# Kernel optimization log

Measured on AMD Instinct MI355X. Metric: run time of the kernel, lower is better.

## Reference

```python
import jax, jax.numpy as jnp
import numpy as np

WINDOW = 5  # pairs (i, j) with j in [i+1, i+5]
NEG = -1e30


def setup_inputs() -> dict:
    key = jax.random.key(0)
    k1, k2, k3, k4 = jax.random.split(key, 4)
    b, l, h = 32, 4096, 768
    words = jax.random.normal(k1, (b, l, h), dtype=jnp.float32)
    diff = jax.random.normal(k2, (b, l), dtype=jnp.float32)  # unused by module
    W = jax.random.normal(k3, (1, 2 * h), dtype=jnp.float32) * (1.0 / np.sqrt(2 * h))
    bias = jax.random.normal(k4, (1,), dtype=jnp.float32) * 0.01
    return {"words": words, "diff": diff, "W": W, "b": bias}


def reference(words, diff, W, b):
    # Original: for each (i, j) with 1 <= j-i <= 5, score = relu(Linear(cat(w_i, w_j)))
    # then max over all pairs -> (batch, 1).
    # Linear factorizes: cat(w_i, w_j) @ W.T = w_i @ w1 + w_j @ w2.
    h = words.shape[-1]
    w1, w2 = W[0, :h], W[0, h:]
    s = jnp.einsum('blh,h->bl', words, w1)  # contribution of left word i
    t = jnp.einsum('blh,h->bl', words, w2)  # contribution of right word j
    # shifted right-contributions for offsets 1..5; pad with NEG so relu -> 0
    # (valid since all real scores are >= 0 after relu and L >= 2)
    shifted = jnp.stack(
        [jnp.pad(t[:, k:], ((0, 0), (0, k)), constant_values=NEG) for k in range(1, WINDOW + 1)],
        axis=-1,
    )  # (b, l, 5)
    scores = jax.nn.relu(s[:, :, None] + shifted + b[0])  # (b, l, 5)
    out = jnp.max(scores.reshape(scores.shape[0], -1), axis=1, keepdims=True)  # (b, 1)
    return out
```

## Files before the change

### kernel.cpp

```cpp
#include <hip/hip_runtime.h>

#define BATCH 32
#define LSEQ  4096
#define HDIM  768
#define NEGV  (-1e30f)

__global__ __launch_bounds__(256) void st_kernel(const float* __restrict__ words,
                                                 const float* __restrict__ W,
                                                 float* __restrict__ s_buf,
                                                 float* __restrict__ t_buf,
                                                 int total_groups) {
    const int lane = threadIdx.x & 63;
    const int sub  = lane & 15;
    const int r    = lane >> 4;
    const int wave_global = blockIdx.x * 4 + (threadIdx.x >> 6);
    const int total_waves = gridDim.x * 4;

    const float4* Wv = (const float4*)W;
    float4 a[12], b[12];
    #pragma unroll
    for (int j = 0; j < 12; ++j) {
        a[j] = Wv[sub + 16 * j];
        b[j] = Wv[192 + sub + 16 * j];
    }

    for (int g = wave_global; g < total_groups; g += total_waves) {
        const int row = g * 4 + r;
        const float4* wp = (const float4*)words + (size_t)row * (HDIM / 4);
        float s = 0.f, t = 0.f;
        #pragma unroll
        for (int j = 0; j < 12; ++j) {
            const float4 x = wp[sub + 16 * j];
            s += x.x * a[j].x; s += x.y * a[j].y; s += x.z * a[j].z; s += x.w * a[j].w;
            t += x.x * b[j].x; t += x.y * b[j].y; t += x.z * b[j].z; t += x.w * b[j].w;
        }
        #pragma unroll
        for (int off = 8; off > 0; off >>= 1) {
            s += __shfl_down(s, off, 16);
            t += __shfl_down(t, off, 16);
        }
        if (sub == 0) {
            s_buf[row] = s;
            t_buf[row] = t;
        }
    }
}

__global__ __launch_bounds__(1024) void max_kernel(const float* __restrict__ s_buf,
                                                   const float* __restrict__ t_buf,
                                                   const float* __restrict__ bias,
                                                   float* __restrict__ out) {
    const int b = blockIdx.x;
    const float* s = s_buf + (size_t)b * LSEQ;
    const float* t = t_buf + (size_t)b * LSEQ;

    float m = NEGV;
    for (int l = threadIdx.x; l < LSEQ; l += 1024) {
        float tm = NEGV;
        #pragma unroll
        for (int k = 1; k <= 5; ++k) {
            if (l + k < LSEQ) tm = fmaxf(tm, t[l + k]);
        }
        m = fmaxf(m, s[l] + tm);
    }
    #pragma unroll
    for (int off = 32; off > 0; off >>= 1) {
        m = fmaxf(m, __shfl_down(m, off, 64));
    }
    __shared__ float red[16];
    if ((threadIdx.x & 63) == 0) red[threadIdx.x >> 6] = m;
    __syncthreads();
    if (threadIdx.x == 0) {
        float M = NEGV;
        #pragma unroll
        for (int i = 0; i < 16; ++i) M = fmaxf(M, red[i]);
        out[b] = fmaxf(0.f, M + bias[0]);
    }
}

extern "C" void kernel_launch(void* const* d_in, const int* in_sizes, int n_in,
                              void* d_out, int out_size, void* d_ws, size_t ws_size,
                              hipStream_t stream) {
    const float* words = (const float*)d_in[0];
    const float* W    = (const float*)d_in[2];
    const float* bias = (const float*)d_in[3];
    float* out = (float*)d_out;

    float* s_buf = (float*)d_ws;
    float* t_buf = s_buf + BATCH * LSEQ;

    const int total_groups = (BATCH * LSEQ) / 4;
    st_kernel<<<2048, 256, 0, stream>>>(words, W, s_buf, t_buf, total_groups);
    max_kernel<<<BATCH, 1024, 0, stream>>>(s_buf, t_buf, bias, out);
}
```

Measured before the change: 528.0 us.

## Use 32-lane row groups with two rows per wave iteration and batched loads

The dot-product kernel now assigns 32 lanes per row with two rows per half-wave per iteration. All 12 float4 loads are issued before any FMA, which raises memory-level parallelism for this bandwidth-bound 400MB read. Block size goes to 512 with a min-blocks hint, and the max kernel drops to 256 threads. The cost is more registers per thread, and the reduction now needs five shuffle steps instead of four.

```diff
diff --git a/kernel.cpp b/kernel.cpp
--- a/kernel.cpp
+++ b/kernel.cpp
@@ -5,57 +5,69 @@
 #define HDIM  768
 #define NEGV  (-1e30f)
 
-__global__ __launch_bounds__(256) void st_kernel(const float* __restrict__ words,
-                                                 const float* __restrict__ W,
-                                                 float* __restrict__ s_buf,
-                                                 float* __restrict__ t_buf,
-                                                 int total_groups) {
+__global__ __launch_bounds__(512, 4) void st_kernel(const float* __restrict__ words,
+                                                    const float* __restrict__ W,
+                                                    float* __restrict__ s_buf,
+                                                    float* __restrict__ t_buf,
+                                                    int total_quads) {
     const int lane = threadIdx.x & 63;
-    const int sub  = lane & 15;
-    const int r    = lane >> 4;
-    const int wave_global = blockIdx.x * 4 + (threadIdx.x >> 6);
-    const int total_waves = gridDim.x * 4;
+    const int sub  = lane & 31;
+    const int r    = lane >> 5;
+    const int wave_global = blockIdx.x * 8 + (threadIdx.x >> 6);
+    const int total_waves = gridDim.x * 8;
 
     const float4* Wv = (const float4*)W;
-    float4 a[12], b[12];
+    float4 a[6], b[6];
     #pragma unroll
-    for (int j = 0; j < 12; ++j) {
-        a[j] = Wv[sub + 16 * j];
-        b[j] = Wv[192 + sub + 16 * j];
+    for (int j = 0; j < 6; ++j) {
+        a[j] = Wv[sub + 32 * j];
+        b[j] = Wv[192 + sub + 32 * j];
     }
 
-    for (int g = wave_global; g < total_groups; g += total_waves) {
-        const int row = g * 4 + r;
-        const float4* wp = (const float4*)words + (size_t)row * (HDIM / 4);
-        float s = 0.f, t = 0.f;
+    for (int q = wave_global; q < total_quads; q += total_waves) {
+        const int row0 = q * 4 + r;
+        const int row1 = row0 + 2;
+        const float4* wp0 = (const float4*)words + (size_t)row0 * (HDIM / 4);
+        const float4* wp1 = (const float4*)words + (size_t)row1 * (HDIM / 4);
+
+        float4 x0[6], x1[6];
         #pragma unroll
-        for (int j = 0; j < 12; ++j) {
-            const float4 x = wp[sub + 16 * j];
-            s += x.x * a[j].x; s += x.y * a[j].y; s += x.z * a[j].z; s += x.w * a[j].w;
-            t += x.x * b[j].x; t += x.y * b[j].y; t += x.z * b[j].z; t += x.w * b[j].w;
+        for (int j = 0; j < 6; ++j) x0[j] = wp0[sub + 32 * j];
+        #pragma unroll
+        for (int j = 0; j < 6; ++j) x1[j] = wp1[sub + 32 * j];
+
+        float s0 = 0.f, t0 = 0.f, s1 = 0.f, t1 = 0.f;
+        #pragma unroll
+        for (int j = 0; j < 6; ++j) {
+            s0 += x0[j].x * a[j].x; s0 += x0[j].y * a[j].y; s0 += x0[j].z * a[j].z; s0 += x0[j].w * a[j].w;
+            t0 += x0[j].x * b[j].x; t0 += x0[j].y * b[j].y; t0 += x0[j].z * b[j].z; t0 += x0[j].w * b[j].w;
+            s1 += x1[j].x * a[j].x; s1 += x1[j].y * a[j].y; s1 += x1[j].z * a[j].z; s1 += x1[j].w * a[j].w;
+            t1 += x1[j].x * b[j].x; t1 += x1[j].y * b[j].y; t1 += x1[j].z * b[j].z; t1 += x1[j].w * b[j].w;
         }
         #pragma unroll
-        for (int off = 8; off > 0; off >>= 1) {
-            s += __shfl_down(s, off, 16);
-            t += __shfl_down(t, off, 16);
+        for (int off = 16; off > 0; off >>= 1) {
+            s0 += __shfl_down(s0, off, 32);
+            t0 += __shfl_down(t0, off, 32);
+            s1 += __shfl_down(s1, off, 32);
+            t1 += __shfl_down(t1, off, 32);
         }
         if (sub == 0) {
-            s_buf[row] = s;
-            t_buf[row] = t;
+            s_buf[row0] = s0;  t_buf[row0] = t0;
+            s_buf[row1] = s1;  t_buf[row1] = t1;
         }
     }
 }
 
-__global__ __launch_bounds__(1024) void max_kernel(const float* __restrict__ s_buf,
-                                                   const float* __restrict__ t_buf,
-                                                   const float* __restrict__ bias,
-                                                   float* __restrict__ out) {
+__global__ __launch_bounds__(256) void max_kernel(const float* __restrict__ s_buf,
+                                                  const float* __restrict__ t_buf,
+                                                  const float* __restrict__ bias,
+                                                  float* __restrict__ out) {
     const int b = blockIdx.x;
     const float* s = s_buf + (size_t)b * LSEQ;
     const float* t = t_buf + (size_t)b * LSEQ;
 
     float m = NEGV;
-    for (int l = threadIdx.x; l < LSEQ; l += 1024) {
+    for (int l = threadIdx.x; l < LSEQ; l += 256) {
         float tm = NEGV;
         #pragma unroll
         for (int k = 1; k <= 5; ++k) {
@@ -67,13 +79,11 @@
     for (int off = 32; off > 0; off >>= 1) {
         m = fmaxf(m, __shfl_down(m, off, 64));
     }
-    __shared__ float red[16];
+    __shared__ float red[4];
     if ((threadIdx.x & 63) == 0) red[threadIdx.x >> 6] = m;
     __syncthreads();
     if (threadIdx.x == 0) {
-        float M = NEGV;
-        #pragma unroll
-        for (int i = 0; i < 16; ++i) M = fmaxf(M, red[i]);
+        float M = fmaxf(fmaxf(red[0], red[1]), fmaxf(red[2], red[3]));
         out[b] = fmaxf(0.f, M + bias[0]);
     }
 }
@@ -89,7 +99,7 @@
     float* s_buf = (float*)d_ws;
     float* t_buf = s_buf + BATCH * LSEQ;
 
-    const int total_groups = (BATCH * LSEQ) / 4;
-    st_kernel<<<2048, 256, 0, stream>>>(words, W, s_buf, t_buf, total_groups);
-    max_kernel<<<BATCH, 1024, 0, stream>>>(s_buf, t_buf, bias, out);
+    const int total_quads = (BATCH * LSEQ) / 4;
+    st_kernel<<<1024, 512, 0, stream>>>(words, W, s_buf, t_buf, total_quads);
+    max_kernel<<<BATCH, 256, 0, stream>>>(s_buf, t_buf, bias, out);
 }
```

New measurement: 543.6 us. +3.0%, slower.
